# Kernel optimization log

Hardware: AMD Instinct MI355X
Metric: run time of the kernel (lower is better)

The kernel has to match this reference:

```python
import jax, jax.numpy as jnp
import numpy as np

NUM_EXPERTS = 64
TOP_K = 8
HIDDEN = 2048
INTER = 768


def setup_inputs() -> dict:
    key = jax.random.key(0)
    k1, k2, k3, k4, k5 = jax.random.split(key, 5)
    hidden_states = jax.random.normal(k1, (4, 256, HIDDEN), dtype=jnp.float32)
    # router gate: Linear(hidden, num_experts, bias=False); stored as [H, E]
    gate_w = jax.random.normal(k2, (HIDDEN, NUM_EXPERTS), dtype=jnp.float32) * 0.02
    # per-expert SwiGLU FFN weights (w13 split into gate/up, plus down)
    w_gate = jax.random.normal(k3, (NUM_EXPERTS, HIDDEN, INTER), dtype=jnp.float32) * 0.02
    w_up = jax.random.normal(k4, (NUM_EXPERTS, HIDDEN, INTER), dtype=jnp.float32) * 0.02
    w_down = jax.random.normal(k5, (NUM_EXPERTS, INTER, HIDDEN), dtype=jnp.float32) * 0.02
    return {"hidden_states": hidden_states, "gate_w": gate_w,
            "w_gate": w_gate, "w_up": w_up, "w_down": w_down}


def reference(hidden_states, gate_w, w_gate, w_up, w_down):
    orig_shape = hidden_states.shape
    x = hidden_states.reshape(-1, orig_shape[-1])          # [T, H]
    T = x.shape[0]
    # router: softmax over expert logits, top-k select, renormalize (norm_topk_prob=True)
    router_logits = x @ gate_w                              # [T, E]
    probs = jax.nn.softmax(router_logits.astype(jnp.float32), axis=-1)
    top_vals, top_idx = jax.lax.top_k(probs, TOP_K)         # [T, K]
    top_vals = top_vals / jnp.sum(top_vals, axis=-1, keepdims=True)
    # dense [T, E] routing-weight matrix (zeros off the top-k) — jit-friendly dispatch
    rw = jnp.zeros((T, NUM_EXPERTS), dtype=x.dtype)
    rw = rw.at[jnp.arange(T)[:, None], top_idx].set(top_vals)
    # SwiGLU expert FFN evaluated per (token, expert), weighted-combined
    g = jnp.einsum('th,ehi->tei', x, w_gate)                # [T, E, I]
    u = jnp.einsum('th,ehi->tei', x, w_up)                  # [T, E, I]
    h = jax.nn.silu(g) * u                                  # [T, E, I]
    h = h * rw[:, :, None]                                  # fold routing weight before down-proj
    out = jnp.einsum('tei,eih->th', h, w_down)              # [T, H]
    return out.reshape(orig_shape)
```

## Files before the change

kernel.cpp:

```cpp
#include <hip/hip_runtime.h>
#include <cstdint>

#define T_TOK 1024
#define HID   2048
#define NEXP  64
#define TOPK  8
#define INTER 768

typedef __attribute__((ext_vector_type(8))) short short8;
typedef __attribute__((ext_vector_type(4))) float f32x4;

__device__ __forceinline__ unsigned short f2bf(float f){
  unsigned u = __float_as_uint(f);
  u += 0x7FFFu + ((u >> 16) & 1u);
  return (unsigned short)(u >> 16);
}

__global__ void k_convert_x(const float* __restrict__ x, unsigned short* __restrict__ xbf){
  int gid = blockIdx.x * 256 + threadIdx.x;
  const float4* src = (const float4*)(x + (size_t)gid * 8);
  float4 a = src[0], b = src[1];
  uint4 p;
  p.x = f2bf(a.x) | ((unsigned)f2bf(a.y) << 16);
  p.y = f2bf(a.z) | ((unsigned)f2bf(a.w) << 16);
  p.z = f2bf(b.x) | ((unsigned)f2bf(b.y) << 16);
  p.w = f2bf(b.z) | ((unsigned)f2bf(b.w) << 16);
  *(uint4*)(xbf + (size_t)gid * 8) = p;
}

__global__ void k_router(const float* __restrict__ x, const float* __restrict__ gw,
                         int* __restrict__ top_idx, float* __restrict__ top_w){
  int t = blockIdx.x;
  int tid = threadIdx.x;
  __shared__ float  xs[HID];
  __shared__ double part[4][NEXP];
  for (int i = tid; i < HID; i += 256) xs[i] = x[(size_t)t * HID + i];
  __syncthreads();
  int e = tid & 63, q = tid >> 6;
  double acc = 0.0;
  const float* gp = gw + e;
  #pragma unroll 8
  for (int h = q * 512; h < q * 512 + 512; ++h)
    acc += (double)xs[h] * (double)gp[(size_t)h * NEXP];
  part[q][e] = acc;
  __syncthreads();
  if (tid < 64){
    float logit = (float)(part[0][e] + part[1][e] + part[2][e] + part[3][e]);
    float cur = logit;
    float vals[TOPK]; int idxs[TOPK];
    #pragma unroll
    for (int k = 0; k < TOPK; ++k){
      float m = cur; int mi = e;
      #pragma unroll
      for (int off = 32; off > 0; off >>= 1){
        float ov = __shfl_xor(m, off);
        int   oi = __shfl_xor(mi, off);
        if (ov > m || (ov == m && oi < mi)){ m = ov; mi = oi; }
      }
      vals[k] = m; idxs[k] = mi;
      if (e == mi) cur = -1e30f;
    }
    float mx = vals[0], s = 0.f, ev[TOPK];
    #pragma unroll
    for (int k = 0; k < TOPK; ++k){ ev[k] = expf(vals[k] - mx); s += ev[k]; }
    #pragma unroll
    for (int k = 0; k < TOPK; ++k)
      if (e == k){ top_idx[t * TOPK + k] = idxs[k]; top_w[t * TOPK + k] = ev[k] / s; }
  }
}

__global__ void k_hist(const int* __restrict__ top_idx, int* __restrict__ offs){
  __shared__ int hist[NEXP];
  int tid = threadIdx.x;
  if (tid < NEXP) hist[tid] = 0;
  __syncthreads();
  for (int j = tid; j < T_TOK * TOPK; j += 256) atomicAdd(&hist[top_idx[j]], 1);
  __syncthreads();
  if (tid == 0){
    int run = 0;
    for (int e = 0; e < NEXP; ++e){ offs[e] = run; run += hist[e]; }
    offs[NEXP] = run;
  }
}

__global__ void k_compact(const int* __restrict__ top_idx, const float* __restrict__ top_w,
                          const int* __restrict__ offs, int* __restrict__ list_t,
                          float* __restrict__ list_w, int* __restrict__ slot_of){
  int e = blockIdx.x, tid = threadIdx.x;
  __shared__ int sc[256];
  int j0 = tid * 32, cnt = 0;
  for (int jj = 0; jj < 32; ++jj) cnt += (top_idx[j0 + jj] == e);
  sc[tid] = cnt; __syncthreads();
  for (int d = 1; d < 256; d <<= 1){
    int v = (tid >= d) ? sc[tid - d] : 0;
    __syncthreads();
    sc[tid] += v;
    __syncthreads();
  }
  int pos = offs[e] + sc[tid] - cnt;
  for (int jj = 0; jj < 32; ++jj){
    int j = j0 + jj;
    if (top_idx[j] == e){
      list_t[pos]  = j >> 3;
      list_w[pos]  = top_w[j];
      slot_of[j]   = pos;
      ++pos;
    }
  }
}

#define BARRIER() do { asm volatile("s_waitcnt lgkmcnt(0)" ::: "memory"); \
                       __builtin_amdgcn_s_barrier(); } while (0)

__global__ __launch_bounds__(512) void k_gateup(
    const unsigned short* __restrict__ xbf, const float* __restrict__ wg,
    const float* __restrict__ wu, const int* __restrict__ offs,
    const int* __restrict__ list_t, const float* __restrict__ list_w,
    unsigned short* __restrict__ act){
  const int KT = HID / 64;
  int e  = blockIdx.y;
  int i0 = blockIdx.x * 64;
  int beg = offs[e], n_e = offs[e + 1] - beg;
  if (n_e <= 0) return;
  int tid = threadIdx.x, lane = tid & 63, wid = tid >> 6;
  int wm = wid & 3, wn = wid >> 2;

  __shared__ unsigned short lB[2][2][64 * 64];

  int bi = tid & 63, bg = tid >> 6;
  int bswz = (bi & 7) << 4;
  const float* gBase = wg + (size_t)e * HID * INTER + i0 + bi;
  const float* uBase = wu + (size_t)e * HID * INTER + i0 + bi;

#define GU_ISSUE_B(t, rg, ru) { \
    const float* _gp = gBase + (size_t)((t) * 64 + bg * 8) * INTER; \
    const float* _up = uBase + (size_t)((t) * 64 + bg * 8) * INTER; \
    _Pragma("unroll") for (int j = 0; j < 8; ++j){ \
      rg[j] = _gp[(size_t)j * INTER]; ru[j] = _up[(size_t)j * INTER]; } }

#define GU_WRITE_B(buf, rg, ru) { \
    uint4 _p; \
    _p.x = f2bf(rg[0]) | ((unsigned)f2bf(rg[1]) << 16); \
    _p.y = f2bf(rg[2]) | ((unsigned)f2bf(rg[3]) << 16); \
    _p.z = f2bf(rg[4]) | ((unsigned)f2bf(rg[5]) << 16); \
    _p.w = f2bf(rg[6]) | ((unsigned)f2bf(rg[7]) << 16); \
    *(uint4*)((char*)&lB[buf][0][0] + bi * 128 + ((bg * 16) ^ bswz)) = _p; \
    _p.x = f2bf(ru[0]) | ((unsigned)f2bf(ru[1]) << 16); \
    _p.y = f2bf(ru[2]) | ((unsigned)f2bf(ru[3]) << 16); \
    _p.z = f2bf(ru[4]) | ((unsigned)f2bf(ru[5]) << 16); \
    _p.w = f2bf(ru[6]) | ((unsigned)f2bf(ru[7]) << 16); \
    *(uint4*)((char*)&lB[buf][1][0] + bi * 128 + ((bg * 16) ^ bswz)) = _p; }

#define GU_ISSUE_A(t, ra) { \
    int _kk = (t) * 64 + ((lane >> 4) << 3); \
    _Pragma("unroll") for (int mf = 0; mf < 3; ++mf){ \
      const unsigned short* _ap = xbf + (size_t)tokA[mf] * HID + _kk; \
      ra[mf][0] = *(const short8*)_ap; \
      ra[mf][1] = *(const short8*)(_ap + 32); } }

#define GU_MFMA(buf, ra) { \
    _Pragma("unroll") for (int ks = 0; ks < 2; ++ks){ \
      short8 _bf[2][2]; \
      _Pragma("unroll") for (int nf = 0; nf < 2; ++nf){ \
        int _il = wn * 32 + nf * 16 + (lane & 15); \
        int _kb = (ks * 64 + ((lane >> 4) << 4)) ^ ((_il & 7) << 4); \
        _bf[0][nf] = *(const short8*)((const char*)&lB[buf][0][0] + _il * 128 + _kb); \
        _bf[1][nf] = *(const short8*)((const char*)&lB[buf][1][0] + _il * 128 + _kb); } \
      _Pragma("unroll") for (int mf = 0; mf < 3; ++mf) \
        _Pragma("unroll") for (int nf = 0; nf < 2; ++nf){ \
          accg[mf][nf] = __builtin_amdgcn_mfma_f32_16x16x32_bf16(ra[mf][ks], _bf[0][nf], accg[mf][nf], 0, 0, 0); \
          accu[mf][nf] = __builtin_amdgcn_mfma_f32_16x16x32_bf16(ra[mf][ks], _bf[1][nf], accu[mf][nf], 0, 0, 0); } } }

  for (int m0 = 0; m0 < n_e; m0 += 192){
    int tokA[3];
    #pragma unroll
    for (int mf = 0; mf < 3; ++mf){
      int r = wm * 48 + mf * 16 + (lane & 15);
      tokA[mf] = list_t[(m0 + r < n_e) ? (beg + m0 + r) : beg];
    }
    float rbg0[8], rbu0[8], rbg1[8], rbu1[8];
    short8 rA0[3][2], rA1[3][2];
    f32x4 accg[3][2] = {}; f32x4 accu[3][2] = {};

    GU_ISSUE_B(0, rbg0, rbu0);
    GU_ISSUE_B(1, rbg1, rbu1);
    GU_ISSUE_A(0, rA0);
    GU_WRITE_B(0, rbg0, rbu0);
    BARRIER();
    #pragma unroll 1
    for (int t = 0; t < KT - 2; t += 2){
      GU_ISSUE_A(t + 1, rA1);
      GU_ISSUE_B(t + 2, rbg0, rbu0);
      GU_MFMA(0, rA0);
      GU_WRITE_B(1, rbg1, rbu1);
      BARRIER();
      GU_ISSUE_A(t + 2, rA0);
      if (t + 3 < KT) { GU_ISSUE_B(t + 3, rbg1, rbu1); }
      GU_MFMA(1, rA1);
      GU_WRITE_B(0, rbg0, rbu0);
      BARRIER();
    }
    GU_ISSUE_A(KT - 1, rA1);
    GU_MFMA(0, rA0);
    GU_WRITE_B(1, rbg1, rbu1);
    BARRIER();
    GU_MFMA(1, rA1);

    #pragma unroll
    for (int mf = 0; mf < 3; ++mf){
      #pragma unroll
      for (int rr = 0; rr < 4; ++rr){
        int r = wm * 48 + mf * 16 + ((lane >> 4) << 2) + rr;
        if (m0 + r < n_e){
          int slot = beg + m0 + r;
          float wgt = list_w[slot];
          #pragma unroll
          for (int nf = 0; nf < 2; ++nf){
            float g = accg[mf][nf][rr], u = accu[mf][nf][rr];
            float h = (g / (1.f + expf(-g))) * u * wgt;
            act[(size_t)slot * INTER + i0 + wn * 32 + nf * 16 + (lane & 15)] = f2bf(h);
          }
        }
      }
    }
    if (m0 + 192 < n_e) BARRIER();
  }
}

__global__ __launch_bounds__(512) void k_down(
    const unsigned short* __restrict__ act, const float* __restrict__ wd,
    const int* __restrict__ offs, const int* __restrict__ list_t,
    float* __restrict__ contrib, float* __restrict__ out, int atomicMode){
  const int KT = INTER / 64;
  int e  = blockIdx.y;
  int n0 = blockIdx.x * 128;
  int beg = offs[e], n_e = offs[e + 1] - beg;
  if (n_e <= 0) return;
  int tid = threadIdx.x, lane = tid & 63, wid = tid >> 6;
  int wm = wid & 3, wn = wid >> 2;

  __shared__ unsigned short lB[2][128 * 64];

  int bh = tid & 127, bg = tid >> 7;
  int hswz = (bh & 7) << 4;
  const float* dBase = wd + (size_t)e * INTER * HID + n0 + bh;

#define DN_ISSUE_B(t, rb) { \
    const float* _p = dBase + (size_t)((t) * 64 + bg * 8) * HID; \
    _Pragma("unroll") for (int j = 0; j < 8; ++j){ \
      rb[j] = _p[(size_t)j * HID]; rb[8 + j] = _p[(size_t)(j + 32) * HID]; } }

#define DN_WRITE_B(buf, rb) { \
    uint4 _p; \
    _p.x = f2bf(rb[0]) | ((unsigned)f2bf(rb[1]) << 16); \
    _p.y = f2bf(rb[2]) | ((unsigned)f2bf(rb[3]) << 16); \
    _p.z = f2bf(rb[4]) | ((unsigned)f2bf(rb[5]) << 16); \
    _p.w = f2bf(rb[6]) | ((unsigned)f2bf(rb[7]) << 16); \
    *(uint4*)((char*)&lB[buf][0] + bh * 128 + ((bg * 16) ^ hswz)) = _p; \
    _p.x = f2bf(rb[8])  | ((unsigned)f2bf(rb[9])  << 16); \
    _p.y = f2bf(rb[10]) | ((unsigned)f2bf(rb[11]) << 16); \
    _p.z = f2bf(rb[12]) | ((unsigned)f2bf(rb[13]) << 16); \
    _p.w = f2bf(rb[14]) | ((unsigned)f2bf(rb[15]) << 16); \
    *(uint4*)((char*)&lB[buf][0] + bh * 128 + ((bg * 16 + 64) ^ hswz)) = _p; }

#define DN_ISSUE_A(t, ra) { \
    int _kk = (t) * 64 + ((lane >> 4) << 3); \
    _Pragma("unroll") for (int mf = 0; mf < 3; ++mf){ \
      const unsigned short* _ap = act + (size_t)aslot[mf] * INTER + _kk; \
      ra[mf][0] = *(const short8*)_ap; \
      ra[mf][1] = *(const short8*)(_ap + 32); } }

#define DN_MFMA(buf, ra) { \
    _Pragma("unroll") for (int ks = 0; ks < 2; ++ks){ \
      short8 _bf[4]; \
      _Pragma("unroll") for (int nf = 0; nf < 4; ++nf){ \
        int _il = wn * 64 + nf * 16 + (lane & 15); \
        int _kb = (ks * 64 + ((lane >> 4) << 4)) ^ ((_il & 7) << 4); \
        _bf[nf] = *(const short8*)((const char*)&lB[buf][0] + _il * 128 + _kb); } \
      _Pragma("unroll") for (int mf = 0; mf < 3; ++mf) \
        _Pragma("unroll") for (int nf = 0; nf < 4; ++nf) \
          acc[mf][nf] = __builtin_amdgcn_mfma_f32_16x16x32_bf16(ra[mf][ks], _bf[nf], acc[mf][nf], 0, 0, 0); } }

  for (int m0 = 0; m0 < n_e; m0 += 192){
    int aslot[3];
    #pragma unroll
    for (int mf = 0; mf < 3; ++mf){
      int r = wm * 48 + mf * 16 + (lane & 15);
      aslot[mf] = (m0 + r < n_e) ? (beg + m0 + r) : beg;
    }
    float rb0[16], rb1[16];
    short8 rA0[3][2], rA1[3][2];
    f32x4 acc[3][4] = {};

    DN_ISSUE_B(0, rb0);
    DN_ISSUE_B(1, rb1);
    DN_ISSUE_A(0, rA0);
    DN_WRITE_B(0, rb0);
    BARRIER();
    #pragma unroll 1
    for (int t = 0; t < KT - 2; t += 2){
      DN_ISSUE_A(t + 1, rA1);
      DN_ISSUE_B(t + 2, rb0);
      DN_MFMA(0, rA0);
      DN_WRITE_B(1, rb1);
      BARRIER();
      DN_ISSUE_A(t + 2, rA0);
      if (t + 3 < KT) { DN_ISSUE_B(t + 3, rb1); }
      DN_MFMA(1, rA1);
      DN_WRITE_B(0, rb0);
      BARRIER();
    }
    DN_ISSUE_A(KT - 1, rA1);
    DN_MFMA(0, rA0);
    DN_WRITE_B(1, rb1);
    BARRIER();
    DN_MFMA(1, rA1);

    #pragma unroll
    for (int mf = 0; mf < 3; ++mf){
      #pragma unroll
      for (int rr = 0; rr < 4; ++rr){
        int r = wm * 48 + mf * 16 + ((lane >> 4) << 2) + rr;
        if (m0 + r < n_e){
          int slot = beg + m0 + r;
          #pragma unroll
          for (int nf = 0; nf < 4; ++nf){
            float v = acc[mf][nf][rr];
            int h = n0 + wn * 64 + nf * 16 + (lane & 15);
            if (atomicMode) atomicAdd(&out[(size_t)list_t[slot] * HID + h], v);
            else            contrib[(size_t)slot * HID + h] = v;
          }
        }
      }
    }
    if (m0 + 192 < n_e) BARRIER();
  }
}

__global__ void k_reduce(const float* __restrict__ contrib, const int* __restrict__ slot_of,
                         float* __restrict__ out){
  int bx = blockIdx.x;
  int t = bx >> 1, seg = bx & 1, tid = threadIdx.x;
  __shared__ int ss[TOPK];
  if (tid < TOPK) ss[tid] = slot_of[t * TOPK + tid];
  __syncthreads();
  int h = (seg * 256 + tid) * 4;
  f32x4 s = {0.f, 0.f, 0.f, 0.f};
  #pragma unroll
  for (int k = 0; k < TOPK; ++k){
    f32x4 v = *(const f32x4*)(contrib + (size_t)ss[k] * HID + h);
    s += v;
  }
  *(f32x4*)(out + (size_t)t * HID + h) = s;
}

extern "C" void kernel_launch(void* const* d_in, const int* in_sizes, int n_in,
                              void* d_out, int out_size, void* d_ws, size_t ws_size,
                              hipStream_t stream){
  const float* x   = (const float*)d_in[0];
  const float* gw  = (const float*)d_in[1];
  const float* wgp = (const float*)d_in[2];
  const float* wup = (const float*)d_in[3];
  const float* wdp = (const float*)d_in[4];
  float* out = (float*)d_out;
  char* ws = (char*)d_ws;

  int*   top_idx = (int*)  (ws + 0);
  float* top_w   = (float*)(ws + 32768);
  int*   offs    = (int*)  (ws + 65536);
  int*   list_t  = (int*)  (ws + 69632);
  float* list_w  = (float*)(ws + 102400);
  int*   slot_of = (int*)  (ws + 135168);
  unsigned short* xbf = (unsigned short*)(ws + 167936);
  unsigned short* act = (unsigned short*)(ws + 167936 + 4194304);
  float* contrib = (float*)(ws + 167936 + 4194304 + 12582912);
  size_t need_full = (size_t)167936 + 4194304 + 12582912 + 67108864;
  int atomicMode = (ws_size < need_full) ? 1 : 0;

  k_convert_x<<<1024, 256, 0, stream>>>(x, xbf);
  k_router   <<<1024, 256, 0, stream>>>(x, gw, top_idx, top_w);
  k_hist     <<<1,    256, 0, stream>>>(top_idx, offs);
  k_compact  <<<64,   256, 0, stream>>>(top_idx, top_w, offs, list_t, list_w, slot_of);
  k_gateup   <<<dim3(INTER / 64, NEXP), 512, 0, stream>>>(xbf, wgp, wup, offs, list_t, list_w, act);
  if (atomicMode){
    hipMemsetAsync(d_out, 0, (size_t)out_size * sizeof(float), stream);
    k_down  <<<dim3(HID / 128, NEXP), 512, 0, stream>>>(act, wdp, offs, list_t, contrib, out, 1);
  } else {
    k_down  <<<dim3(HID / 128, NEXP), 512, 0, stream>>>(act, wdp, offs, list_t, contrib, out, 0);
    k_reduce<<<2048, 256, 0, stream>>>(contrib, slot_of, out);
  }
}
```

Measured before the change: 391.3 us.

## Deepen weight prefetch to triple-buffered LDS and remap expert block order

Both expert GEMM kernels move from a double-buffered LDS pipeline to three LDS stages with three register staging sets. Weight loads are now issued four k-tiles ahead and the loop is fully unrolled into a rotating schedule. The grid is flattened so consecutive blocks cycle across groups of eight experts, `__launch_bounds__(512, 2)` requests two blocks per CU, and a redundant trailing barrier is dropped. The aim is to hide fp32 weight-streaming latency and raise occupancy, at the risk of register spills under the tighter VGPR budget and higher LDS use.

Result: slower. 735.4 us (+87.9%).

```diff
diff --git a/kernel.cpp b/kernel.cpp
--- a/kernel.cpp
+++ b/kernel.cpp
@@ -112,53 +112,55 @@
 #define BARRIER() do { asm volatile("s_waitcnt lgkmcnt(0)" ::: "memory"); \
                        __builtin_amdgcn_s_barrier(); } while (0)
 
-__global__ __launch_bounds__(512) void k_gateup(
+__global__ __launch_bounds__(512, 2) void k_gateup(
     const unsigned short* __restrict__ xbf, const float* __restrict__ wg,
     const float* __restrict__ wu, const int* __restrict__ offs,
     const int* __restrict__ list_t, const float* __restrict__ list_w,
     unsigned short* __restrict__ act){
   const int KT = HID / 64;
-  int e  = blockIdx.y;
-  int i0 = blockIdx.x * 64;
+  int owner = blockIdx.x;
+  int hi = owner >> 3;
+  int e  = (owner & 7) + ((hi / 12) << 3);
+  int i0 = (hi % 12) * 64;
   int beg = offs[e], n_e = offs[e + 1] - beg;
   if (n_e <= 0) return;
   int tid = threadIdx.x, lane = tid & 63, wid = tid >> 6;
   int wm = wid & 3, wn = wid >> 2;
 
-  __shared__ unsigned short lB[2][2][64 * 64];
+  __shared__ unsigned short lB[3][2][64 * 64];
 
   int bi = tid & 63, bg = tid >> 6;
   int bswz = (bi & 7) << 4;
   const float* gBase = wg + (size_t)e * HID * INTER + i0 + bi;
   const float* uBase = wu + (size_t)e * HID * INTER + i0 + bi;
 
-#define GU_ISSUE_B(t, rg, ru) { \
+#define GU_ISSUE_B(t, rg_, ru_) { \
     const float* _gp = gBase + (size_t)((t) * 64 + bg * 8) * INTER; \
     const float* _up = uBase + (size_t)((t) * 64 + bg * 8) * INTER; \
     _Pragma("unroll") for (int j = 0; j < 8; ++j){ \
-      rg[j] = _gp[(size_t)j * INTER]; ru[j] = _up[(size_t)j * INTER]; } }
-
-#define GU_WRITE_B(buf, rg, ru) { \
+      rg_[j] = _gp[(size_t)j * INTER]; ru_[j] = _up[(size_t)j * INTER]; } }
+
+#define GU_WRITE_B(buf, rg_, ru_) { \
     uint4 _p; \
-    _p.x = f2bf(rg[0]) | ((unsigned)f2bf(rg[1]) << 16); \
-    _p.y = f2bf(rg[2]) | ((unsigned)f2bf(rg[3]) << 16); \
-    _p.z = f2bf(rg[4]) | ((unsigned)f2bf(rg[5]) << 16); \
-    _p.w = f2bf(rg[6]) | ((unsigned)f2bf(rg[7]) << 16); \
+    _p.x = f2bf(rg_[0]) | ((unsigned)f2bf(rg_[1]) << 16); \
+    _p.y = f2bf(rg_[2]) | ((unsigned)f2bf(rg_[3]) << 16); \
+    _p.z = f2bf(rg_[4]) | ((unsigned)f2bf(rg_[5]) << 16); \
+    _p.w = f2bf(rg_[6]) | ((unsigned)f2bf(rg_[7]) << 16); \
     *(uint4*)((char*)&lB[buf][0][0] + bi * 128 + ((bg * 16) ^ bswz)) = _p; \
-    _p.x = f2bf(ru[0]) | ((unsigned)f2bf(ru[1]) << 16); \
-    _p.y = f2bf(ru[2]) | ((unsigned)f2bf(ru[3]) << 16); \
-    _p.z = f2bf(ru[4]) | ((unsigned)f2bf(ru[5]) << 16); \
-    _p.w = f2bf(ru[6]) | ((unsigned)f2bf(ru[7]) << 16); \
+    _p.x = f2bf(ru_[0]) | ((unsigned)f2bf(ru_[1]) << 16); \
+    _p.y = f2bf(ru_[2]) | ((unsigned)f2bf(ru_[3]) << 16); \
+    _p.z = f2bf(ru_[4]) | ((unsigned)f2bf(ru_[5]) << 16); \
+    _p.w = f2bf(ru_[6]) | ((unsigned)f2bf(ru_[7]) << 16); \
     *(uint4*)((char*)&lB[buf][1][0] + bi * 128 + ((bg * 16) ^ bswz)) = _p; }
 
-#define GU_ISSUE_A(t, ra) { \
+#define GU_ISSUE_A(t, ra_) { \
     int _kk = (t) * 64 + ((lane >> 4) << 3); \
     _Pragma("unroll") for (int mf = 0; mf < 3; ++mf){ \
       const unsigned short* _ap = xbf + (size_t)tokA[mf] * HID + _kk; \
-      ra[mf][0] = *(const short8*)_ap; \
-      ra[mf][1] = *(const short8*)(_ap + 32); } }
-
-#define GU_MFMA(buf, ra) { \
+      ra_[mf][0] = *(const short8*)_ap; \
+      ra_[mf][1] = *(const short8*)(_ap + 32); } }
+
+#define GU_MFMA(buf, ra_) { \
     _Pragma("unroll") for (int ks = 0; ks < 2; ++ks){ \
       short8 _bf[2][2]; \
       _Pragma("unroll") for (int nf = 0; nf < 2; ++nf){ \
@@ -168,8 +170,15 @@
         _bf[1][nf] = *(const short8*)((const char*)&lB[buf][1][0] + _il * 128 + _kb); } \
       _Pragma("unroll") for (int mf = 0; mf < 3; ++mf) \
         _Pragma("unroll") for (int nf = 0; nf < 2; ++nf){ \
-          accg[mf][nf] = __builtin_amdgcn_mfma_f32_16x16x32_bf16(ra[mf][ks], _bf[0][nf], accg[mf][nf], 0, 0, 0); \
-          accu[mf][nf] = __builtin_amdgcn_mfma_f32_16x16x32_bf16(ra[mf][ks], _bf[1][nf], accu[mf][nf], 0, 0, 0); } } }
+          accg[mf][nf] = __builtin_amdgcn_mfma_f32_16x16x32_bf16(ra_[mf][ks], _bf[0][nf], accg[mf][nf], 0, 0, 0); \
+          accu[mf][nf] = __builtin_amdgcn_mfma_f32_16x16x32_bf16(ra_[mf][ks], _bf[1][nf], accu[mf][nf], 0, 0, 0); } } }
+
+#define GU_BODY(T, ACUR, ANXT, SI, SW, LR, LW, DO_A, DO_B, DO_W) { \
+    if (DO_A) GU_ISSUE_A((T) + 1, rA[ANXT]); \
+    if (DO_B) GU_ISSUE_B((T) + 4, rg[SI], ru[SI]); \
+    GU_MFMA(LR, rA[ACUR]); \
+    if (DO_W) GU_WRITE_B(LW, rg[SW], ru[SW]); \
+    BARRIER(); }
 
   for (int m0 = 0; m0 < n_e; m0 += 192){
     int tokA[3];
@@ -178,33 +187,36 @@
       int r = wm * 48 + mf * 16 + (lane & 15);
       tokA[mf] = list_t[(m0 + r < n_e) ? (beg + m0 + r) : beg];
     }
-    float rbg0[8], rbu0[8], rbg1[8], rbu1[8];
-    short8 rA0[3][2], rA1[3][2];
+    float rg[3][8], ru[3][8];
+    short8 rA[2][3][2];
     f32x4 accg[3][2] = {}; f32x4 accu[3][2] = {};
 
-    GU_ISSUE_B(0, rbg0, rbu0);
-    GU_ISSUE_B(1, rbg1, rbu1);
-    GU_ISSUE_A(0, rA0);
-    GU_WRITE_B(0, rbg0, rbu0);
+    GU_ISSUE_B(0, rg[0], ru[0]);
+    GU_ISSUE_B(1, rg[1], ru[1]);
+    GU_ISSUE_B(2, rg[2], ru[2]);
+    GU_ISSUE_A(0, rA[0]);
+    GU_WRITE_B(0, rg[0], ru[0]);
+    GU_WRITE_B(1, rg[1], ru[1]);
+    GU_ISSUE_B(3, rg[0], ru[0]);
     BARRIER();
+
     #pragma unroll 1
-    for (int t = 0; t < KT - 2; t += 2){
-      GU_ISSUE_A(t + 1, rA1);
-      GU_ISSUE_B(t + 2, rbg0, rbu0);
-      GU_MFMA(0, rA0);
-      GU_WRITE_B(1, rbg1, rbu1);
-      BARRIER();
-      GU_ISSUE_A(t + 2, rA0);
-      if (t + 3 < KT) { GU_ISSUE_B(t + 3, rbg1, rbu1); }
-      GU_MFMA(1, rA1);
-      GU_WRITE_B(0, rbg0, rbu0);
-      BARRIER();
-    }
-    GU_ISSUE_A(KT - 1, rA1);
-    GU_MFMA(0, rA0);
-    GU_WRITE_B(1, rbg1, rbu1);
-    BARRIER();
-    GU_MFMA(1, rA1);
+    for (int t = 0; t < 24; t += 6){
+      GU_BODY(t + 0, 0, 1, 1, 2, 0, 2, 1, 1, 1);
+      GU_BODY(t + 1, 1, 0, 2, 0, 1, 0, 1, 1, 1);
+      GU_BODY(t + 2, 0, 1, 0, 1, 2, 1, 1, 1, 1);
+      GU_BODY(t + 3, 1, 0, 1, 2, 0, 2, 1, 1, 1);
+      GU_BODY(t + 4, 0, 1, 2, 0, 1, 0, 1, 1, 1);
+      GU_BODY(t + 5, 1, 0, 0, 1, 2, 1, 1, 1, 1);
+    }
+    GU_BODY(24, 0, 1, 1, 2, 0, 2, 1, 1, 1);
+    GU_BODY(25, 1, 0, 2, 0, 1, 0, 1, 1, 1);
+    GU_BODY(26, 0, 1, 0, 1, 2, 1, 1, 1, 1);
+    GU_BODY(27, 1, 0, 1, 2, 0, 2, 1, 1, 1);
+    GU_BODY(28, 0, 1, 2, 0, 1, 0, 1, 0, 1);
+    GU_BODY(29, 1, 0, 0, 1, 2, 1, 1, 0, 1);
+    GU_BODY(30, 0, 1, 1, 2, 0, 2, 1, 0, 0);
+    GU_BODY(31, 1, 0, 2, 0, 1, 0, 0, 0, 0);
 
     #pragma unroll
     for (int mf = 0; mf < 3; ++mf){
@@ -223,54 +235,55 @@
         }
       }
     }
-    if (m0 + 192 < n_e) BARRIER();
-  }
-}
-
-__global__ __launch_bounds__(512) void k_down(
+  }
+}
+
+__global__ __launch_bounds__(512, 2) void k_down(
     const unsigned short* __restrict__ act, const float* __restrict__ wd,
     const int* __restrict__ offs, const int* __restrict__ list_t,
     float* __restrict__ contrib, float* __restrict__ out, int atomicMode){
   const int KT = INTER / 64;
-  int e  = blockIdx.y;
-  int n0 = blockIdx.x * 128;
+  int owner = blockIdx.x;
+  int hi = owner >> 3;
+  int e  = (owner & 7) + ((hi >> 4) << 3);
+  int n0 = (hi & 15) * 128;
   int beg = offs[e], n_e = offs[e + 1] - beg;
   if (n_e <= 0) return;
   int tid = threadIdx.x, lane = tid & 63, wid = tid >> 6;
   int wm = wid & 3, wn = wid >> 2;
 
-  __shared__ unsigned short lB[2][128 * 64];
+  __shared__ unsigned short lB[3][128 * 64];
 
   int bh = tid & 127, bg = tid >> 7;
   int hswz = (bh & 7) << 4;
   const float* dBase = wd + (size_t)e * INTER * HID + n0 + bh;
 
-#define DN_ISSUE_B(t, rb) { \
+#define DN_ISSUE_B(t, rb_) { \
     const float* _p = dBase + (size_t)((t) * 64 + bg * 8) * HID; \
     _Pragma("unroll") for (int j = 0; j < 8; ++j){ \
-      rb[j] = _p[(size_t)j * HID]; rb[8 + j] = _p[(size_t)(j + 32) * HID]; } }
-
-#define DN_WRITE_B(buf, rb) { \
+      rb_[j] = _p[(size_t)j * HID]; rb_[8 + j] = _p[(size_t)(j + 32) * HID]; } }
+
+#define DN_WRITE_B(buf, rb_) { \
     uint4 _p; \
-    _p.x = f2bf(rb[0]) | ((unsigned)f2bf(rb[1]) << 16); \
-    _p.y = f2bf(rb[2]) | ((unsigned)f2bf(rb[3]) << 16); \
-    _p.z = f2bf(rb[4]) | ((unsigned)f2bf(rb[5]) << 16); \
-    _p.w = f2bf(rb[6]) | ((unsigned)f2bf(rb[7]) << 16); \
+    _p.x = f2bf(rb_[0]) | ((unsigned)f2bf(rb_[1]) << 16); \
+    _p.y = f2bf(rb_[2]) | ((unsigned)f2bf(rb_[3]) << 16); \
+    _p.z = f2bf(rb_[4]) | ((unsigned)f2bf(rb_[5]) << 16); \
+    _p.w = f2bf(rb_[6]) | ((unsigned)f2bf(rb_[7]) << 16); \
     *(uint4*)((char*)&lB[buf][0] + bh * 128 + ((bg * 16) ^ hswz)) = _p; \
-    _p.x = f2bf(rb[8])  | ((unsigned)f2bf(rb[9])  << 16); \
-    _p.y = f2bf(rb[10]) | ((unsigned)f2bf(rb[11]) << 16); \
-    _p.z = f2bf(rb[12]) | ((unsigned)f2bf(rb[13]) << 16); \
-    _p.w = f2bf(rb[14]) | ((unsigned)f2bf(rb[15]) << 16); \
+    _p.x = f2bf(rb_[8])  | ((unsigned)f2bf(rb_[9])  << 16); \
+    _p.y = f2bf(rb_[10]) | ((unsigned)f2bf(rb_[11]) << 16); \
+    _p.z = f2bf(rb_[12]) | ((unsigned)f2bf(rb_[13]) << 16); \
+    _p.w = f2bf(rb_[14]) | ((unsigned)f2bf(rb_[15]) << 16); \
     *(uint4*)((char*)&lB[buf][0] + bh * 128 + ((bg * 16 + 64) ^ hswz)) = _p; }
 
-#define DN_ISSUE_A(t, ra) { \
+#define DN_ISSUE_A(t, ra_) { \
     int _kk = (t) * 64 + ((lane >> 4) << 3); \
     _Pragma("unroll") for (int mf = 0; mf < 3; ++mf){ \
       const unsigned short* _ap = act + (size_t)aslot[mf] * INTER + _kk; \
-      ra[mf][0] = *(const short8*)_ap; \
-      ra[mf][1] = *(const short8*)(_ap + 32); } }
-
-#define DN_MFMA(buf, ra) { \
+      ra_[mf][0] = *(const short8*)_ap; \
+      ra_[mf][1] = *(const short8*)(_ap + 32); } }
+
+#define DN_MFMA(buf, ra_) { \
     _Pragma("unroll") for (int ks = 0; ks < 2; ++ks){ \
       short8 _bf[4]; \
       _Pragma("unroll") for (int nf = 0; nf < 4; ++nf){ \
@@ -279,7 +292,14 @@
         _bf[nf] = *(const short8*)((const char*)&lB[buf][0] + _il * 128 + _kb); } \
       _Pragma("unroll") for (int mf = 0; mf < 3; ++mf) \
         _Pragma("unroll") for (int nf = 0; nf < 4; ++nf) \
-          acc[mf][nf] = __builtin_amdgcn_mfma_f32_16x16x32_bf16(ra[mf][ks], _bf[nf], acc[mf][nf], 0, 0, 0); } }
+          acc[mf][nf] = __builtin_amdgcn_mfma_f32_16x16x32_bf16(ra_[mf][ks], _bf[nf], acc[mf][nf], 0, 0, 0); } }
+
+#define DN_BODY(T, ACUR, ANXT, SI, SW, LR, LW, DO_A, DO_B, DO_W) { \
+    if (DO_A) DN_ISSUE_A((T) + 1, rA[ANXT]); \
+    if (DO_B) DN_ISSUE_B((T) + 4, rb[SI]); \
+    DN_MFMA(LR, rA[ACUR]); \
+    if (DO_W) DN_WRITE_B(LW, rb[SW]); \
+    BARRIER(); }
 
   for (int m0 = 0; m0 < n_e; m0 += 192){
     int aslot[3];
@@ -288,33 +308,31 @@
       int r = wm * 48 + mf * 16 + (lane & 15);
       aslot[mf] = (m0 + r < n_e) ? (beg + m0 + r) : beg;
     }
-    float rb0[16], rb1[16];
-    short8 rA0[3][2], rA1[3][2];
+    float rb[3][16];
+    short8 rA[2][3][2];
     f32x4 acc[3][4] = {};
 
-    DN_ISSUE_B(0, rb0);
-    DN_ISSUE_B(1, rb1);
-    DN_ISSUE_A(0, rA0);
-    DN_WRITE_B(0, rb0);
+    DN_ISSUE_B(0, rb[0]);
+    DN_ISSUE_B(1, rb[1]);
+    DN_ISSUE_B(2, rb[2]);
+    DN_ISSUE_A(0, rA[0]);
+    DN_WRITE_B(0, rb[0]);
+    DN_WRITE_B(1, rb[1]);
+    DN_ISSUE_B(3, rb[0]);
     BARRIER();
-    #pragma unroll 1
-    for (int t = 0; t < KT - 2; t += 2){
-      DN_ISSUE_A(t + 1, rA1);
-      DN_ISSUE_B(t + 2, rb0);
-      DN_MFMA(0, rA0);
-      DN_WRITE_B(1, rb1);
-      BARRIER();
-      DN_ISSUE_A(t + 2, rA0);
-      if (t + 3 < KT) { DN_ISSUE_B(t + 3, rb1); }
-      DN_MFMA(1, rA1);
-      DN_WRITE_B(0, rb0);
-      BARRIER();
-    }
-    DN_ISSUE_A(KT - 1, rA1);
-    DN_MFMA(0, rA0);
-    DN_WRITE_B(1, rb1);
-    BARRIER();
-    DN_MFMA(1, rA1);
+
+    DN_BODY(0,  0, 1, 1, 2, 0, 2, 1, 1, 1);
+    DN_BODY(1,  1, 0, 2, 0, 1, 0, 1, 1, 1);
+    DN_BODY(2,  0, 1, 0, 1, 2, 1, 1, 1, 1);
+    DN_BODY(3,  1, 0, 1, 2, 0, 2, 1, 1, 1);
+    DN_BODY(4,  0, 1, 2, 0, 1, 0, 1, 1, 1);
+    DN_BODY(5,  1, 0, 0, 1, 2, 1, 1, 1, 1);
+    DN_BODY(6,  0, 1, 1, 2, 0, 2, 1, 1, 1);
+    DN_BODY(7,  1, 0, 2, 0, 1, 0, 1, 1, 1);
+    DN_BODY(8,  0, 1, 0, 1, 2, 1, 1, 0, 1);
+    DN_BODY(9,  1, 0, 1, 2, 0, 2, 1, 0, 1);
+    DN_BODY(10, 0, 1, 2, 0, 1, 0, 1, 0, 0);
+    DN_BODY(11, 1, 0, 0, 1, 2, 1, 0, 0, 0);
 
     #pragma unroll
     for (int mf = 0; mf < 3; ++mf){
@@ -333,7 +351,6 @@
         }
       }
     }
-    if (m0 + 192 < n_e) BARRIER();
   }
 }
 
@@ -381,12 +398,12 @@
   k_router   <<<1024, 256, 0, stream>>>(x, gw, top_idx, top_w);
   k_hist     <<<1,    256, 0, stream>>>(top_idx, offs);
   k_compact  <<<64,   256, 0, stream>>>(top_idx, top_w, offs, list_t, list_w, slot_of);
-  k_gateup   <<<dim3(INTER / 64, NEXP), 512, 0, stream>>>(xbf, wgp, wup, offs, list_t, list_w, act);
+  k_gateup   <<<dim3(12 * NEXP), 512, 0, stream>>>(xbf, wgp, wup, offs, list_t, list_w, act);
   if (atomicMode){
     hipMemsetAsync(d_out, 0, (size_t)out_size * sizeof(float), stream);
-    k_down  <<<dim3(HID / 128, NEXP), 512, 0, stream>>>(act, wdp, offs, list_t, contrib, out, 1);
+    k_down  <<<dim3(16 * NEXP), 512, 0, stream>>>(act, wdp, offs, list_t, contrib, out, 1);
   } else {
-    k_down  <<<dim3(HID / 128, NEXP), 512, 0, stream>>>(act, wdp, offs, list_t, contrib, out, 0);
+    k_down  <<<dim3(16 * NEXP), 512, 0, stream>>>(act, wdp, offs, list_t, contrib, out, 0);
     k_reduce<<<2048, 256, 0, stream>>>(contrib, slot_of, out);
   }
 }
```

## Stage expert weights via global_load_lds into a 4-deep fp32 LDS ring

Applied to the files above, without the earlier changes.

Both expert GEMM kernels now copy fp32 weight tiles straight from global memory into LDS with direct-to-LDS 16-byte loads, using a 4-stage ring buffer with vmcnt-based waits. Previously each thread loaded the tiles into registers, converted them to bf16 and wrote them to LDS. The bf16 conversion now happens when the MFMA operands are read from LDS, which means more scalar LDS reads and repeated conversion work per wave. In exchange it frees registers and allows deeper prefetch. Token ids and routing weights are also cached in shared memory per 192-row tile, which adds extra __syncthreads.

Measured after the change: 541.3 us. 38.3% more time.

```diff
diff --git a/kernel.cpp b/kernel.cpp
--- a/kernel.cpp
+++ b/kernel.cpp
@@ -109,15 +109,18 @@
   }
 }
 
-#define BARRIER() do { asm volatile("s_waitcnt lgkmcnt(0)" ::: "memory"); \
-                       __builtin_amdgcn_s_barrier(); } while (0)
+#define GLL16(SRC, DST) \
+  __builtin_amdgcn_global_load_lds((const __attribute__((address_space(1))) unsigned int*)(SRC), \
+                                   (__attribute__((address_space(3))) unsigned int*)(DST), 16, 0, 0)
+
+#define WAITV(N) do { asm volatile("s_waitcnt vmcnt(" #N ")" ::: "memory"); \
+                      __builtin_amdgcn_s_barrier(); } while (0)
 
 __global__ __launch_bounds__(512) void k_gateup(
     const unsigned short* __restrict__ xbf, const float* __restrict__ wg,
     const float* __restrict__ wu, const int* __restrict__ offs,
     const int* __restrict__ list_t, const float* __restrict__ list_w,
     unsigned short* __restrict__ act){
-  const int KT = HID / 64;
   int e  = blockIdx.y;
   int i0 = blockIdx.x * 64;
   int beg = offs[e], n_e = offs[e + 1] - beg;
@@ -125,86 +128,90 @@
   int tid = threadIdx.x, lane = tid & 63, wid = tid >> 6;
   int wm = wid & 3, wn = wid >> 2;
 
-  __shared__ unsigned short lB[2][2][64 * 64];
-
-  int bi = tid & 63, bg = tid >> 6;
-  int bswz = (bi & 7) << 4;
-  const float* gBase = wg + (size_t)e * HID * INTER + i0 + bi;
-  const float* uBase = wu + (size_t)e * HID * INTER + i0 + bi;
-
-#define GU_ISSUE_B(t, rg, ru) { \
-    const float* _gp = gBase + (size_t)((t) * 64 + bg * 8) * INTER; \
-    const float* _up = uBase + (size_t)((t) * 64 + bg * 8) * INTER; \
-    _Pragma("unroll") for (int j = 0; j < 8; ++j){ \
-      rg[j] = _gp[(size_t)j * INTER]; ru[j] = _up[(size_t)j * INTER]; } }
-
-#define GU_WRITE_B(buf, rg, ru) { \
-    uint4 _p; \
-    _p.x = f2bf(rg[0]) | ((unsigned)f2bf(rg[1]) << 16); \
-    _p.y = f2bf(rg[2]) | ((unsigned)f2bf(rg[3]) << 16); \
-    _p.z = f2bf(rg[4]) | ((unsigned)f2bf(rg[5]) << 16); \
-    _p.w = f2bf(rg[6]) | ((unsigned)f2bf(rg[7]) << 16); \
-    *(uint4*)((char*)&lB[buf][0][0] + bi * 128 + ((bg * 16) ^ bswz)) = _p; \
-    _p.x = f2bf(ru[0]) | ((unsigned)f2bf(ru[1]) << 16); \
-    _p.y = f2bf(ru[2]) | ((unsigned)f2bf(ru[3]) << 16); \
-    _p.z = f2bf(ru[4]) | ((unsigned)f2bf(ru[5]) << 16); \
-    _p.w = f2bf(ru[6]) | ((unsigned)f2bf(ru[7]) << 16); \
-    *(uint4*)((char*)&lB[buf][1][0] + bi * 128 + ((bg * 16) ^ bswz)) = _p; }
-
-#define GU_ISSUE_A(t, ra) { \
-    int _kk = (t) * 64 + ((lane >> 4) << 3); \
+  __shared__ float lB[4][2][64 * 64];
+  __shared__ int   sTok[192];
+  __shared__ float sWgt[192];
+
+  const float* gBase = wg + (size_t)e * HID * INTER + i0;
+  const float* uBase = wu + (size_t)e * HID * INTER + i0;
+
+#define GU_STAGE(T) { \
+    float* _base = &lB[(T) & 3][0][0]; \
+    _Pragma("unroll") for (int jj = 0; jj < 4; ++jj){ \
+      int _idx = wid * 4 + jj;                \
+      int _mat = _idx >> 4, _q16 = _idx & 15; \
+      int _s = (_q16 >> 1) & 1; \
+      int _row = (T) * 64 + _q16 * 4 + (lane >> 4); \
+      const float* _src = (_mat ? uBase : gBase) + (size_t)_row * INTER \
+                          + (((lane & 15) ^ (_s << 2)) << 2); \
+      float* _dst = _base + _mat * 4096 + _q16 * 256 + lane * 4; \
+      GLL16(_src, _dst); } }
+
+#define GU_ISSUE_A(T, ra_) { \
+    int _kk = (T) * 64 + ((lane >> 4) << 3); \
     _Pragma("unroll") for (int mf = 0; mf < 3; ++mf){ \
       const unsigned short* _ap = xbf + (size_t)tokA[mf] * HID + _kk; \
-      ra[mf][0] = *(const short8*)_ap; \
-      ra[mf][1] = *(const short8*)(_ap + 32); } }
-
-#define GU_MFMA(buf, ra) { \
+      ra_[mf][0] = *(const short8*)_ap; \
+      ra_[mf][1] = *(const short8*)(_ap + 32); } }
+
+#define GU_MFMA_PHASE(T, ra_) { \
+    const char* _lg = (const char*)&lB[(T) & 3][0][0]; \
+    const char* _lu = (const char*)&lB[(T) & 3][1][0]; \
+    int _c = lane & 15, _kq = lane >> 4; \
     _Pragma("unroll") for (int ks = 0; ks < 2; ++ks){ \
-      short8 _bf[2][2]; \
+      short8 _bg[2], _bu[2]; \
       _Pragma("unroll") for (int nf = 0; nf < 2; ++nf){ \
-        int _il = wn * 32 + nf * 16 + (lane & 15); \
-        int _kb = (ks * 64 + ((lane >> 4) << 4)) ^ ((_il & 7) << 4); \
-        _bf[0][nf] = *(const short8*)((const char*)&lB[buf][0][0] + _il * 128 + _kb); \
-        _bf[1][nf] = *(const short8*)((const char*)&lB[buf][1][0] + _il * 128 + _kb); } \
+        int _col = wn * 32 + nf * 16 + _c; \
+        int _off0 = ((((_col >> 2) ^ ((_kq & 1) << 2)) << 4) + ((_col & 3) << 2)); \
+        union { uint4 u; short8 s; } _vg, _vu; \
+        _Pragma("unroll") for (int jp = 0; jp < 4; ++jp){ \
+          int _k0 = ks * 32 + _kq * 8 + jp * 2; \
+          int _a0 = ((_k0 >> 2) << 10) + ((_k0 & 3) << 8) + _off0; \
+          int _a1 = _a0 + 256; \
+          float _g0 = *(const float*)(_lg + _a0), _g1 = *(const float*)(_lg + _a1); \
+          float _u0 = *(const float*)(_lu + _a0), _u1 = *(const float*)(_lu + _a1); \
+          ((unsigned*)&_vg)[jp] = f2bf(_g0) | ((unsigned)f2bf(_g1) << 16); \
+          ((unsigned*)&_vu)[jp] = f2bf(_u0) | ((unsigned)f2bf(_u1) << 16); } \
+        _bg[nf] = _vg.s; _bu[nf] = _vu.s; } \
       _Pragma("unroll") for (int mf = 0; mf < 3; ++mf) \
         _Pragma("unroll") for (int nf = 0; nf < 2; ++nf){ \
-          accg[mf][nf] = __builtin_amdgcn_mfma_f32_16x16x32_bf16(ra[mf][ks], _bf[0][nf], accg[mf][nf], 0, 0, 0); \
-          accu[mf][nf] = __builtin_amdgcn_mfma_f32_16x16x32_bf16(ra[mf][ks], _bf[1][nf], accu[mf][nf], 0, 0, 0); } } }
+          accg[mf][nf] = __builtin_amdgcn_mfma_f32_16x16x32_bf16(ra_[mf][ks], _bg[nf], accg[mf][nf], 0, 0, 0); \
+          accu[mf][nf] = __builtin_amdgcn_mfma_f32_16x16x32_bf16(ra_[mf][ks], _bu[nf], accu[mf][nf], 0, 0, 0); } } }
+
+#define GU_BODY(T, RAc, RAn) { \
+    GU_ISSUE_A((T) + 1, RAn); \
+    GU_STAGE((T) + 3); \
+    GU_MFMA_PHASE(T, RAc); \
+    WAITV(4); }
 
   for (int m0 = 0; m0 < n_e; m0 += 192){
+    __syncthreads();
+    if (tid < 192){
+      int sl = beg + m0 + tid;
+      if (m0 + tid < n_e){ sTok[tid] = list_t[sl]; sWgt[tid] = list_w[sl]; }
+      else               { sTok[tid] = list_t[beg]; sWgt[tid] = 0.f; }
+    }
+    __syncthreads();
     int tokA[3];
     #pragma unroll
-    for (int mf = 0; mf < 3; ++mf){
-      int r = wm * 48 + mf * 16 + (lane & 15);
-      tokA[mf] = list_t[(m0 + r < n_e) ? (beg + m0 + r) : beg];
-    }
-    float rbg0[8], rbu0[8], rbg1[8], rbu1[8];
+    for (int mf = 0; mf < 3; ++mf) tokA[mf] = sTok[wm * 48 + mf * 16 + (lane & 15)];
+
     short8 rA0[3][2], rA1[3][2];
     f32x4 accg[3][2] = {}; f32x4 accu[3][2] = {};
 
-    GU_ISSUE_B(0, rbg0, rbu0);
-    GU_ISSUE_B(1, rbg1, rbu1);
     GU_ISSUE_A(0, rA0);
-    GU_WRITE_B(0, rbg0, rbu0);
-    BARRIER();
+    GU_STAGE(0); GU_STAGE(1); GU_STAGE(2);
+    WAITV(8);
+
     #pragma unroll 1
-    for (int t = 0; t < KT - 2; t += 2){
-      GU_ISSUE_A(t + 1, rA1);
-      GU_ISSUE_B(t + 2, rbg0, rbu0);
-      GU_MFMA(0, rA0);
-      GU_WRITE_B(1, rbg1, rbu1);
-      BARRIER();
-      GU_ISSUE_A(t + 2, rA0);
-      if (t + 3 < KT) { GU_ISSUE_B(t + 3, rbg1, rbu1); }
-      GU_MFMA(1, rA1);
-      GU_WRITE_B(0, rbg0, rbu0);
-      BARRIER();
-    }
-    GU_ISSUE_A(KT - 1, rA1);
-    GU_MFMA(0, rA0);
-    GU_WRITE_B(1, rbg1, rbu1);
-    BARRIER();
-    GU_MFMA(1, rA1);
+    for (int t = 0; t < 28; t += 2){
+      GU_BODY(t,     rA0, rA1);
+      GU_BODY(t + 1, rA1, rA0);
+    }
+    GU_BODY(28, rA0, rA1);
+    { GU_ISSUE_A(30, rA0); GU_MFMA_PHASE(29, rA1); WAITV(0); }
+    { GU_ISSUE_A(31, rA1); GU_MFMA_PHASE(30, rA0); WAITV(0); }
+    GU_MFMA_PHASE(31, rA1);
 
     #pragma unroll
     for (int mf = 0; mf < 3; ++mf){
@@ -213,7 +220,7 @@
         int r = wm * 48 + mf * 16 + ((lane >> 4) << 2) + rr;
         if (m0 + r < n_e){
           int slot = beg + m0 + r;
-          float wgt = list_w[slot];
+          float wgt = sWgt[r];
           #pragma unroll
           for (int nf = 0; nf < 2; ++nf){
             float g = accg[mf][nf][rr], u = accu[mf][nf][rr];
@@ -223,7 +230,6 @@
         }
       }
     }
-    if (m0 + 192 < n_e) BARRIER();
   }
 }
 
@@ -231,7 +237,6 @@
     const unsigned short* __restrict__ act, const float* __restrict__ wd,
     const int* __restrict__ offs, const int* __restrict__ list_t,
     float* __restrict__ contrib, float* __restrict__ out, int atomicMode){
-  const int KT = INTER / 64;
   int e  = blockIdx.y;
   int n0 = blockIdx.x * 128;
   int beg = offs[e], n_e = offs[e + 1] - beg;
@@ -239,82 +244,83 @@
   int tid = threadIdx.x, lane = tid & 63, wid = tid >> 6;
   int wm = wid & 3, wn = wid >> 2;
 
-  __shared__ unsigned short lB[2][128 * 64];
-
-  int bh = tid & 127, bg = tid >> 7;
-  int hswz = (bh & 7) << 4;
-  const float* dBase = wd + (size_t)e * INTER * HID + n0 + bh;
-
-#define DN_ISSUE_B(t, rb) { \
-    const float* _p = dBase + (size_t)((t) * 64 + bg * 8) * HID; \
-    _Pragma("unroll") for (int j = 0; j < 8; ++j){ \
-      rb[j] = _p[(size_t)j * HID]; rb[8 + j] = _p[(size_t)(j + 32) * HID]; } }
-
-#define DN_WRITE_B(buf, rb) { \
-    uint4 _p; \
-    _p.x = f2bf(rb[0]) | ((unsigned)f2bf(rb[1]) << 16); \
-    _p.y = f2bf(rb[2]) | ((unsigned)f2bf(rb[3]) << 16); \
-    _p.z = f2bf(rb[4]) | ((unsigned)f2bf(rb[5]) << 16); \
-    _p.w = f2bf(rb[6]) | ((unsigned)f2bf(rb[7]) << 16); \
-    *(uint4*)((char*)&lB[buf][0] + bh * 128 + ((bg * 16) ^ hswz)) = _p; \
-    _p.x = f2bf(rb[8])  | ((unsigned)f2bf(rb[9])  << 16); \
-    _p.y = f2bf(rb[10]) | ((unsigned)f2bf(rb[11]) << 16); \
-    _p.z = f2bf(rb[12]) | ((unsigned)f2bf(rb[13]) << 16); \
-    _p.w = f2bf(rb[14]) | ((unsigned)f2bf(rb[15]) << 16); \
-    *(uint4*)((char*)&lB[buf][0] + bh * 128 + ((bg * 16 + 64) ^ hswz)) = _p; }
-
-#define DN_ISSUE_A(t, ra) { \
-    int _kk = (t) * 64 + ((lane >> 4) << 3); \
+  __shared__ float lB[4][64 * 128];
+  __shared__ int   sTok[192];
+
+  const float* dBase = wd + (size_t)e * INTER * HID + n0;
+
+#define DN_STAGE(T) { \
+    float* _base = &lB[(T) & 3][0]; \
+    _Pragma("unroll") for (int jj = 0; jj < 4; ++jj){ \
+      int _idx = wid * 4 + jj;                \
+      int _s = (_idx >> 2) & 1; \
+      int _row = (T) * 64 + _idx * 2 + (lane >> 5); \
+      const float* _src = dBase + (size_t)_row * HID + (((lane & 31) ^ (_s << 2)) << 2); \
+      float* _dst = _base + _idx * 256 + lane * 4; \
+      GLL16(_src, _dst); } }
+
+#define DN_ISSUE_A(T, ra_) { \
+    int _kk = (T) * 64 + ((lane >> 4) << 3); \
     _Pragma("unroll") for (int mf = 0; mf < 3; ++mf){ \
       const unsigned short* _ap = act + (size_t)aslot[mf] * INTER + _kk; \
-      ra[mf][0] = *(const short8*)_ap; \
-      ra[mf][1] = *(const short8*)(_ap + 32); } }
-
-#define DN_MFMA(buf, ra) { \
+      ra_[mf][0] = *(const short8*)_ap; \
+      ra_[mf][1] = *(const short8*)(_ap + 32); } }
+
+#define DN_MFMA_PHASE(T, ra_) { \
+    const char* _lb = (const char*)&lB[(T) & 3][0]; \
+    int _c = lane & 15, _kq = lane >> 4; \
     _Pragma("unroll") for (int ks = 0; ks < 2; ++ks){ \
       short8 _bf[4]; \
       _Pragma("unroll") for (int nf = 0; nf < 4; ++nf){ \
-        int _il = wn * 64 + nf * 16 + (lane & 15); \
-        int _kb = (ks * 64 + ((lane >> 4) << 4)) ^ ((_il & 7) << 4); \
-        _bf[nf] = *(const short8*)((const char*)&lB[buf][0] + _il * 128 + _kb); } \
+        int _col = wn * 64 + nf * 16 + _c; \
+        int _off0 = ((((_col >> 2) ^ ((_kq & 1) << 2)) << 4) + ((_col & 3) << 2)); \
+        union { uint4 u; short8 s; } _vb; \
+        _Pragma("unroll") for (int jp = 0; jp < 4; ++jp){ \
+          int _kh = ks * 16 + _kq * 4 + jp;    \
+          int _a0 = (_kh << 10) + _off0; \
+          float _b0 = *(const float*)(_lb + _a0); \
+          float _b1 = *(const float*)(_lb + _a0 + 512); \
+          ((unsigned*)&_vb)[jp] = f2bf(_b0) | ((unsigned)f2bf(_b1) << 16); } \
+        _bf[nf] = _vb.s; } \
       _Pragma("unroll") for (int mf = 0; mf < 3; ++mf) \
         _Pragma("unroll") for (int nf = 0; nf < 4; ++nf) \
-          acc[mf][nf] = __builtin_amdgcn_mfma_f32_16x16x32_bf16(ra[mf][ks], _bf[nf], acc[mf][nf], 0, 0, 0); } }
+          acc[mf][nf] = __builtin_amdgcn_mfma_f32_16x16x32_bf16(ra_[mf][ks], _bf[nf], acc[mf][nf], 0, 0, 0); } }
+
+#define DN_BODY(T, RAc, RAn) { \
+    DN_ISSUE_A((T) + 1, RAn); \
+    DN_STAGE((T) + 3); \
+    DN_MFMA_PHASE(T, RAc); \
+    WAITV(4); }
 
   for (int m0 = 0; m0 < n_e; m0 += 192){
+    __syncthreads();
+    if (tid < 192){
+      int sl = beg + m0 + tid;
+      sTok[tid] = (m0 + tid < n_e) ? list_t[sl] : 0;
+    }
+    __syncthreads();
     int aslot[3];
     #pragma unroll
     for (int mf = 0; mf < 3; ++mf){
       int r = wm * 48 + mf * 16 + (lane & 15);
       aslot[mf] = (m0 + r < n_e) ? (beg + m0 + r) : beg;
     }
-    float rb0[16], rb1[16];
     short8 rA0[3][2], rA1[3][2];
     f32x4 acc[3][4] = {};
 
-    DN_ISSUE_B(0, rb0);
-    DN_ISSUE_B(1, rb1);
     DN_ISSUE_A(0, rA0);
-    DN_WRITE_B(0, rb0);
-    BARRIER();
+    DN_STAGE(0); DN_STAGE(1); DN_STAGE(2);
+    WAITV(8);
+
     #pragma unroll 1
-    for (int t = 0; t < KT - 2; t += 2){
-      DN_ISSUE_A(t + 1, rA1);
-      DN_ISSUE_B(t + 2, rb0);
-      DN_MFMA(0, rA0);
-      DN_WRITE_B(1, rb1);
-      BARRIER();
-      DN_ISSUE_A(t + 2, rA0);
-      if (t + 3 < KT) { DN_ISSUE_B(t + 3, rb1); }
-      DN_MFMA(1, rA1);
-      DN_WRITE_B(0, rb0);
-      BARRIER();
-    }
-    DN_ISSUE_A(KT - 1, rA1);
-    DN_MFMA(0, rA0);
-    DN_WRITE_B(1, rb1);
-    BARRIER();
-    DN_MFMA(1, rA1);
+    for (int t = 0; t < 8; t += 2){
+      DN_BODY(t,     rA0, rA1);
+      DN_BODY(t + 1, rA1, rA0);
+    }
+    DN_BODY(8, rA0, rA1);
+    { DN_ISSUE_A(10, rA0); DN_MFMA_PHASE(9,  rA1); WAITV(0); }
+    { DN_ISSUE_A(11, rA1); DN_MFMA_PHASE(10, rA0); WAITV(0); }
+    DN_MFMA_PHASE(11, rA1);
 
     #pragma unroll
     for (int mf = 0; mf < 3; ++mf){
@@ -327,13 +333,12 @@
           for (int nf = 0; nf < 4; ++nf){
             float v = acc[mf][nf][rr];
             int h = n0 + wn * 64 + nf * 16 + (lane & 15);
-            if (atomicMode) atomicAdd(&out[(size_t)list_t[slot] * HID + h], v);
+            if (atomicMode) atomicAdd(&out[(size_t)sTok[r] * HID + h], v);
             else            contrib[(size_t)slot * HID + h] = v;
           }
         }
       }
     }
-    if (m0 + 192 < n_e) BARRIER();
   }
 }
 
```
